# Performance work log

Measured on AMD Instinct MI355X. Metric: run time of the kernel, lower is better.

Reference implementation:

```python
import jax, jax.numpy as jnp
import numpy as np

T, B, I, H = 2048, 64, 256, 256

def setup_inputs() -> dict:
    key = jax.random.key(0)
    ks = jax.random.split(key, 9)
    s = 1.0 / np.sqrt(H)  # PyTorch RNN init scale (uniform(-s, s))
    u = lambda k, shape: jax.random.uniform(k, shape, jnp.float32, -s, s)
    return {
        "x": jax.random.normal(ks[0], (T, B, I), jnp.float32),
        "W_ih0": u(ks[1], (H, I)), "W_hh0": u(ks[2], (H, H)),
        "b_ih0": u(ks[3], (H,)),   "b_hh0": u(ks[4], (H,)),
        "W_ih1": u(ks[5], (H, H)), "W_hh1": u(ks[6], (H, H)),
        "b_ih1": u(ks[7], (H,)),   "b_hh1": u(ks[8], (H,)),
    }

def _rnn_layer(x, W_ih, W_hh, b_ih, b_hh):
    # x: [T, B, Din] -> [T, B, H]; h_t = tanh(x_t W_ih^T + b_ih + h_{t-1} W_hh^T + b_hh)
    xp = jnp.einsum('tbi,hi->tbh', x, W_ih) + (b_ih + b_hh)  # precompute input GEMM
    h0 = jnp.zeros((x.shape[1], W_hh.shape[0]), x.dtype)
    def step(h, xt):
        h = jnp.tanh(xt + h @ W_hh.T)
        return h, h
    _, ys = jax.lax.scan(step, h0, xp)
    return ys

def reference(x, W_ih0, W_hh0, b_ih0, b_hh0, W_ih1, W_hh1, b_ih1, b_hh1):
    h1 = _rnn_layer(x, W_ih0, W_hh0, b_ih0, b_hh0)
    h2 = _rnn_layer(h1, W_ih1, W_hh1, b_ih1, b_hh1)
    return h2.reshape(-1, H)  # [T*B, H], matching out.view(-1, hidden_size)
```

## Files before the change

kernel.cpp:

```cpp
#include <hip/hip_runtime.h>
#include <cstdint>

#define T_STEPS 2048
#define HID 256

typedef _Float16 half8 __attribute__((ext_vector_type(8)));
typedef float f32x4 __attribute__((ext_vector_type(4)));

__device__ __forceinline__ float tanh_fast(float x){
  float e = __builtin_amdgcn_exp2f(x * 2.8853900817779268f);
  float r = __builtin_amdgcn_rcpf(e + 1.0f);
  return __builtin_fmaf(-2.0f, r, 1.0f);
}

__device__ __forceinline__ half8 cvt_frag8(const float* __restrict__ p){
  float4 a = *(const float4*)p;
  float4 b = *(const float4*)(p + 4);
  half8 h;
  h[0]=(_Float16)a.x; h[1]=(_Float16)a.y; h[2]=(_Float16)a.z; h[3]=(_Float16)a.w;
  h[4]=(_Float16)b.x; h[5]=(_Float16)b.y; h[6]=(_Float16)b.z; h[7]=(_Float16)b.w;
  return h;
}

__global__ __launch_bounds__(512, 2) void gemm_xp0(
    const float* __restrict__ x, const float* __restrict__ W,
    const float* __restrict__ b1, const float* __restrict__ b2,
    _Float16* __restrict__ xp)
{
  const int t = blockIdx.x, tid = threadIdx.x;
  const int gw = tid >> 6, l = tid & 63;
  const int ng = gw & 1, mg = gw >> 1;
  const int lm = l & 15, lq = l >> 4;

  half8 Af[4][8];
  #pragma unroll
  for (int mt4 = 0; mt4 < 4; ++mt4)
    #pragma unroll
    for (int kc = 0; kc < 8; ++kc)
      Af[mt4][kc] = cvt_frag8(W + (long)(mg*64 + mt4*16 + lm)*HID + kc*32 + lq*8);

  half8 Bf[2][8];
  #pragma unroll
  for (int nt = 0; nt < 2; ++nt)
    #pragma unroll
    for (int kc = 0; kc < 8; ++kc)
      Bf[nt][kc] = cvt_frag8(x + ((long)t*64 + ng*32 + nt*16 + lm)*HID + kc*32 + lq*8);

  f32x4 acc[4][2];
  #pragma unroll
  for (int mt4 = 0; mt4 < 4; ++mt4)
    #pragma unroll
    for (int nt = 0; nt < 2; ++nt)
      acc[mt4][nt] = (f32x4){0.f,0.f,0.f,0.f};

  #pragma unroll
  for (int kc = 0; kc < 8; ++kc)
    #pragma unroll
    for (int mt4 = 0; mt4 < 4; ++mt4)
      #pragma unroll
      for (int nt = 0; nt < 2; ++nt)
        acc[mt4][nt] = __builtin_amdgcn_mfma_f32_16x16x32_f16(
            Af[mt4][kc], Bf[nt][kc], acc[mt4][nt], 0, 0, 0);

  _Float16* chunk0 = xp + ((long)t*4 + ng*2)*4096;
  #pragma unroll
  for (int wp = 0; wp < 2; ++wp){
    const int h0a = mg*64 + (2*wp    )*16 + lq*4;
    const int h0b = mg*64 + (2*wp + 1)*16 + lq*4;
    float4 ba1 = *(const float4*)(b1 + h0a), ba2 = *(const float4*)(b2 + h0a);
    float4 bb1 = *(const float4*)(b1 + h0b), bb2 = *(const float4*)(b2 + h0b);
    #pragma unroll
    for (int nt = 0; nt < 2; ++nt){
      f32x4 v0 = acc[2*wp][nt], v1 = acc[2*wp+1][nt];
      union { _Float16 h[8]; uint4 u; } pk;
      pk.h[0]=(_Float16)(v0[0]+ba1.x+ba2.x); pk.h[1]=(_Float16)(v0[1]+ba1.y+ba2.y);
      pk.h[2]=(_Float16)(v0[2]+ba1.z+ba2.z); pk.h[3]=(_Float16)(v0[3]+ba1.w+ba2.w);
      pk.h[4]=(_Float16)(v1[0]+bb1.x+bb2.x); pk.h[5]=(_Float16)(v1[1]+bb1.y+bb2.y);
      pk.h[6]=(_Float16)(v1[2]+bb1.z+bb2.z); pk.h[7]=(_Float16)(v1[3]+bb1.w+bb2.w);
      *(uint4*)(chunk0 + nt*4096 + ((mg*2 + wp)*64 + l)*8) = pk.u;
    }
  }
}

__global__ __launch_bounds__(512, 2) void fused_rec(
    const _Float16* __restrict__ xp,
    const float* __restrict__ Whh0, const float* __restrict__ Wih1,
    const float* __restrict__ Whh1,
    const float* __restrict__ b1, const float* __restrict__ b2,
    _Float16* __restrict__ hout)
{
  __shared__ __align__(16) _Float16 h1b[2][16][264];
  __shared__ __align__(16) _Float16 h2b[2][16][264];
  const int bi = blockIdx.x, tid = threadIdx.x;
  const int w = tid >> 6, l = tid & 63;
  const int lm = l & 15, lq = l >> 4;

  for (int i = tid; i < 16*264; i += 512){
    (&h1b[1][0][0])[i] = (_Float16)0.f;
    (&h2b[1][0][0])[i] = (_Float16)0.f;
  }

  half8 A0[2][8], A1[2][8], A2[2][8];
  #pragma unroll
  for (int mt = 0; mt < 2; ++mt)
    #pragma unroll
    for (int kc = 0; kc < 8; ++kc){
      const long r = (long)(w*32 + mt*16 + lm)*HID + kc*32 + lq*8;
      A0[mt][kc] = cvt_frag8(Whh0 + r);
      A1[mt][kc] = cvt_frag8(Wih1 + r);
      A2[mt][kc] = cvt_frag8(Whh1 + r);
    }

  f32x4 biasf[2];
  #pragma unroll
  for (int mt = 0; mt < 2; ++mt){
    const int h0 = w*32 + mt*16 + lq*4;
    f32x4 b;
    b[0]=b1[h0+0]+b2[h0+0]; b[1]=b1[h0+1]+b2[h0+1];
    b[2]=b1[h0+2]+b2[h0+2]; b[3]=b1[h0+3]+b2[h0+3];
    biasf[mt] = b;
  }
  __syncthreads();

  const _Float16* xptr = xp + (long)bi*4096 + (w*64 + l)*8;
  uint4 xv = *(const uint4*)xptr;
  _Float16* hob = hout + ((long)bi*16 + lm)*HID + w*32 + lq*4;

  for (int t = 0; t < T_STEPS; ++t){
    const int pb = (t + 1) & 1, cb = t & 1;

    union { uint4 u; _Float16 h[8]; } xu; xu.u = xv;
    f32x4 a0, a1;
    a0[0]=(float)xu.h[0]; a0[1]=(float)xu.h[1]; a0[2]=(float)xu.h[2]; a0[3]=(float)xu.h[3];
    a1[0]=(float)xu.h[4]; a1[1]=(float)xu.h[5]; a1[2]=(float)xu.h[6]; a1[3]=(float)xu.h[7];

    if (t + 1 < T_STEPS){ xptr += 4*4096; xv = *(const uint4*)xptr; }

    #pragma unroll
    for (int kc = 0; kc < 8; ++kc){
      half8 B = *(const half8*)&h1b[pb][lm][kc*32 + lq*8];
      a0 = __builtin_amdgcn_mfma_f32_16x16x32_f16(A0[0][kc], B, a0, 0,0,0);
      a1 = __builtin_amdgcn_mfma_f32_16x16x32_f16(A0[1][kc], B, a1, 0,0,0);
    }

    {
      union { _Float16 h[4]; uint64_t u; } p0, p1;
      p0.h[0]=(_Float16)tanh_fast(a0[0]); p0.h[1]=(_Float16)tanh_fast(a0[1]);
      p0.h[2]=(_Float16)tanh_fast(a0[2]); p0.h[3]=(_Float16)tanh_fast(a0[3]);
      p1.h[0]=(_Float16)tanh_fast(a1[0]); p1.h[1]=(_Float16)tanh_fast(a1[1]);
      p1.h[2]=(_Float16)tanh_fast(a1[2]); p1.h[3]=(_Float16)tanh_fast(a1[3]);
      *(uint64_t*)&h1b[cb][lm][w*32      + lq*4] = p0.u;
      *(uint64_t*)&h1b[cb][lm][w*32 + 16 + lq*4] = p1.u;
    }
    __syncthreads();

    a0 = biasf[0]; a1 = biasf[1];
    #pragma unroll
    for (int kc = 0; kc < 8; ++kc){
      half8 B = *(const half8*)&h1b[cb][lm][kc*32 + lq*8];
      a0 = __builtin_amdgcn_mfma_f32_16x16x32_f16(A1[0][kc], B, a0, 0,0,0);
      a1 = __builtin_amdgcn_mfma_f32_16x16x32_f16(A1[1][kc], B, a1, 0,0,0);
    }
    #pragma unroll
    for (int kc = 0; kc < 8; ++kc){
      half8 B = *(const half8*)&h2b[pb][lm][kc*32 + lq*8];
      a0 = __builtin_amdgcn_mfma_f32_16x16x32_f16(A2[0][kc], B, a0, 0,0,0);
      a1 = __builtin_amdgcn_mfma_f32_16x16x32_f16(A2[1][kc], B, a1, 0,0,0);
    }

    {
      union { _Float16 h[4]; uint64_t u; } q0, q1;
      q0.h[0]=(_Float16)tanh_fast(a0[0]); q0.h[1]=(_Float16)tanh_fast(a0[1]);
      q0.h[2]=(_Float16)tanh_fast(a0[2]); q0.h[3]=(_Float16)tanh_fast(a0[3]);
      q1.h[0]=(_Float16)tanh_fast(a1[0]); q1.h[1]=(_Float16)tanh_fast(a1[1]);
      q1.h[2]=(_Float16)tanh_fast(a1[2]); q1.h[3]=(_Float16)tanh_fast(a1[3]);
      *(uint64_t*)&h2b[cb][lm][w*32      + lq*4] = q0.u;
      *(uint64_t*)&h2b[cb][lm][w*32 + 16 + lq*4] = q1.u;
      _Float16* o = hob + (long)t*64*HID;
      *(uint64_t*)o        = q0.u;
      *(uint64_t*)(o + 16) = q1.u;
    }
    __syncthreads();
  }
}

__global__ __launch_bounds__(256) void cvt_out(
    const _Float16* __restrict__ hin, float* __restrict__ out)
{
  const long i = ((long)blockIdx.x*256 + threadIdx.x)*8;
  half8 v = *(const half8*)(hin + i);
  float4 a, b;
  a.x=(float)v[0]; a.y=(float)v[1]; a.z=(float)v[2]; a.w=(float)v[3];
  b.x=(float)v[4]; b.y=(float)v[5]; b.z=(float)v[6]; b.w=(float)v[7];
  *(float4*)(out + i)     = a;
  *(float4*)(out + i + 4) = b;
}

extern "C" void kernel_launch(void* const* d_in, const int* in_sizes, int n_in,
                              void* d_out, int out_size, void* d_ws, size_t ws_size,
                              hipStream_t stream)
{
  const float* x     = (const float*)d_in[0];
  const float* W_ih0 = (const float*)d_in[1];
  const float* W_hh0 = (const float*)d_in[2];
  const float* b_ih0 = (const float*)d_in[3];
  const float* b_hh0 = (const float*)d_in[4];
  const float* W_ih1 = (const float*)d_in[5];
  const float* W_hh1 = (const float*)d_in[6];
  const float* b_ih1 = (const float*)d_in[7];
  const float* b_hh1 = (const float*)d_in[8];

  _Float16* xp0 = (_Float16*)d_out;
  _Float16* h2  = (_Float16*)d_ws;

  gemm_xp0<<<T_STEPS, 512, 0, stream>>>(x, W_ih0, b_ih0, b_hh0, xp0);
  fused_rec<<<4, 512, 0, stream>>>(xp0, W_hh0, W_ih1, W_hh1, b_ih1, b_hh1, h2);
  cvt_out<<<(T_STEPS*64*HID)/(256*8), 256, 0, stream>>>(h2, (float*)d_out);
}
```

Baseline: 3.574 ms.

## Split the two RNN layers into producer/consumer blocks pipelined through global-memory flags

The fused recurrence kernel is split across 8 blocks. Blocks 0-3 run layer 0 only: four warps compute the recurrence while four others publish each step's hidden state into the spent xp slot and set a release flag. Blocks 4-7 run layer 1, spin on the flag and prefetch the next layer-0 state. The aim is to overlap the two serial recurrences instead of running both per step in one block, which shortens the per-step critical path. The cost is cross-block spin-wait synchronisation, and progress relies on all 8 blocks being resident at the same time.

```diff
diff --git a/kernel.cpp b/kernel.cpp
--- a/kernel.cpp
+++ b/kernel.cpp
@@ -3,6 +3,7 @@
 
 #define T_STEPS 2048
 #define HID 256
+#define TSTRIDE 16384
 
 typedef _Float16 half8 __attribute__((ext_vector_type(8)));
 typedef float f32x4 __attribute__((ext_vector_type(4)));
@@ -82,105 +83,184 @@
   }
 }
 
-__global__ __launch_bounds__(512, 2) void fused_rec(
-    const _Float16* __restrict__ xp,
+__global__ __launch_bounds__(512, 2) void fused_pipe(
+    _Float16* __restrict__ xp,
     const float* __restrict__ Whh0, const float* __restrict__ Wih1,
     const float* __restrict__ Whh1,
     const float* __restrict__ b1, const float* __restrict__ b2,
+    unsigned long long* __restrict__ flags,
     _Float16* __restrict__ hout)
 {
-  __shared__ __align__(16) _Float16 h1b[2][16][264];
-  __shared__ __align__(16) _Float16 h2b[2][16][264];
-  const int bi = blockIdx.x, tid = threadIdx.x;
+  __shared__ __align__(16) _Float16 hsb[2][16][264];
+  const int tid = threadIdx.x;
   const int w = tid >> 6, l = tid & 63;
   const int lm = l & 15, lq = l >> 4;
 
-  for (int i = tid; i < 16*264; i += 512){
-    (&h1b[1][0][0])[i] = (_Float16)0.f;
-    (&h2b[1][0][0])[i] = (_Float16)0.f;
-  }
-
-  half8 A0[2][8], A1[2][8], A2[2][8];
-  #pragma unroll
-  for (int mt = 0; mt < 2; ++mt)
+  for (int i = tid; i < 16*264; i += 512) (&hsb[1][0][0])[i] = (_Float16)0.f;
+
+  if (blockIdx.x < 4) {
+    const int bi = blockIdx.x;
+    unsigned long long* flag = flags + (size_t)bi*16;
+    _Float16* chunk0 = xp + (size_t)bi*4096;
+
+    if (w < 4) {
+      half8 A0[4][8];
+      #pragma unroll
+      for (int mt = 0; mt < 4; ++mt)
+        #pragma unroll
+        for (int kc = 0; kc < 8; ++kc)
+          A0[mt][kc] = cvt_frag8(Whh0 + (size_t)(w*64 + mt*16 + lm)*HID + kc*32 + lq*8);
+      __syncthreads();
+
+      uint4 xva = *(const uint4*)(chunk0 + ((2*w    )*64 + l)*8);
+      uint4 xvb = *(const uint4*)(chunk0 + ((2*w + 1)*64 + l)*8);
+
+      for (int t = 0; t <= T_STEPS; ++t){
+        const int pb = (t + 1) & 1, cb = t & 1;
+        if (t < T_STEPS){
+          union { uint4 u; _Float16 h[8]; } xa, xb;
+          xa.u = xva; xb.u = xvb;
+          f32x4 acc[4];
+          acc[0][0]=(float)xa.h[0]; acc[0][1]=(float)xa.h[1]; acc[0][2]=(float)xa.h[2]; acc[0][3]=(float)xa.h[3];
+          acc[1][0]=(float)xa.h[4]; acc[1][1]=(float)xa.h[5]; acc[1][2]=(float)xa.h[6]; acc[1][3]=(float)xa.h[7];
+          acc[2][0]=(float)xb.h[0]; acc[2][1]=(float)xb.h[1]; acc[2][2]=(float)xb.h[2]; acc[2][3]=(float)xb.h[3];
+          acc[3][0]=(float)xb.h[4]; acc[3][1]=(float)xb.h[5]; acc[3][2]=(float)xb.h[6]; acc[3][3]=(float)xb.h[7];
+
+          if (t + 1 < T_STEPS){
+            const _Float16* nx = chunk0 + (size_t)(t+1)*TSTRIDE;
+            xva = *(const uint4*)(nx + ((2*w    )*64 + l)*8);
+            xvb = *(const uint4*)(nx + ((2*w + 1)*64 + l)*8);
+          }
+
+          #pragma unroll
+          for (int kc = 0; kc < 8; ++kc){
+            half8 B = *(const half8*)&hsb[pb][lm][kc*32 + lq*8];
+            acc[0] = __builtin_amdgcn_mfma_f32_16x16x32_f16(A0[0][kc], B, acc[0], 0,0,0);
+            acc[1] = __builtin_amdgcn_mfma_f32_16x16x32_f16(A0[1][kc], B, acc[1], 0,0,0);
+            acc[2] = __builtin_amdgcn_mfma_f32_16x16x32_f16(A0[2][kc], B, acc[2], 0,0,0);
+            acc[3] = __builtin_amdgcn_mfma_f32_16x16x32_f16(A0[3][kc], B, acc[3], 0,0,0);
+          }
+
+          #pragma unroll
+          for (int mt = 0; mt < 4; ++mt){
+            union { _Float16 h[4]; unsigned long long u; } p;
+            p.h[0]=(_Float16)tanh_fast(acc[mt][0]); p.h[1]=(_Float16)tanh_fast(acc[mt][1]);
+            p.h[2]=(_Float16)tanh_fast(acc[mt][2]); p.h[3]=(_Float16)tanh_fast(acc[mt][3]);
+            *(unsigned long long*)&hsb[cb][lm][w*64 + mt*16 + lq*4] = p.u;
+          }
+        }
+        __syncthreads();
+      }
+    } else {
+      __syncthreads();
+      const int kcA = w - 4;
+      for (int t = 0; t <= T_STEPS; ++t){
+        const int pb = (t + 1) & 1;
+        if (t > 0){
+          union { half8 h; unsigned long long q[2]; } fa, fb;
+          fa.h = *(const half8*)&hsb[pb][lm][kcA*32 + lq*8];
+          fb.h = *(const half8*)&hsb[pb][lm][(kcA+4)*32 + lq*8];
+          _Float16* slot = chunk0 + (size_t)(t-1)*TSTRIDE;
+          unsigned long long* dA = (unsigned long long*)(slot + ((size_t)kcA*64 + l)*8);
+          unsigned long long* dB = (unsigned long long*)(slot + ((size_t)(kcA+4)*64 + l)*8);
+          __hip_atomic_store(dA,   fa.q[0], __ATOMIC_RELAXED, __HIP_MEMORY_SCOPE_AGENT);
+          __hip_atomic_store(dA+1, fa.q[1], __ATOMIC_RELAXED, __HIP_MEMORY_SCOPE_AGENT);
+          __hip_atomic_store(dB,   fb.q[0], __ATOMIC_RELAXED, __HIP_MEMORY_SCOPE_AGENT);
+          __hip_atomic_store(dB+1, fb.q[1], __ATOMIC_RELAXED, __HIP_MEMORY_SCOPE_AGENT);
+        }
+        __syncthreads();
+        if (tid == 256 && t > 0)
+          __hip_atomic_store(flag, (unsigned long long)t,
+                             __ATOMIC_RELEASE, __HIP_MEMORY_SCOPE_AGENT);
+      }
+    }
+  } else {
+    const int bi = blockIdx.x - 4;
+    const unsigned long long* flag = flags + (size_t)bi*16;
+    const _Float16* chunk0 = xp + (size_t)bi*4096;
+
+    half8 A1[2][8], A2[2][8];
+    #pragma unroll
+    for (int mt = 0; mt < 2; ++mt)
+      #pragma unroll
+      for (int kc = 0; kc < 8; ++kc){
+        const size_t r = (size_t)(w*32 + mt*16 + lm)*HID + kc*32 + lq*8;
+        A1[mt][kc] = cvt_frag8(Wih1 + r);
+        A2[mt][kc] = cvt_frag8(Whh1 + r);
+      }
+    f32x4 biasf[2];
+    #pragma unroll
+    for (int mt = 0; mt < 2; ++mt){
+      const int h0 = w*32 + mt*16 + lq*4;
+      f32x4 b;
+      b[0]=b1[h0+0]+b2[h0+0]; b[1]=b1[h0+1]+b2[h0+1];
+      b[2]=b1[h0+2]+b2[h0+2]; b[3]=b1[h0+3]+b2[h0+3];
+      biasf[mt] = b;
+    }
+    __syncthreads();
+    _Float16* hob = hout + ((size_t)bi*16 + lm)*HID + w*32 + lq*4;
+
+    while (__hip_atomic_load(flag, __ATOMIC_ACQUIRE, __HIP_MEMORY_SCOPE_AGENT) < 1ull)
+      __builtin_amdgcn_s_sleep(2);
+    half8 pfc[8], pfn[8];
     #pragma unroll
     for (int kc = 0; kc < 8; ++kc){
-      const long r = (long)(w*32 + mt*16 + lm)*HID + kc*32 + lq*8;
-      A0[mt][kc] = cvt_frag8(Whh0 + r);
-      A1[mt][kc] = cvt_frag8(Wih1 + r);
-      A2[mt][kc] = cvt_frag8(Whh1 + r);
-    }
-
-  f32x4 biasf[2];
-  #pragma unroll
-  for (int mt = 0; mt < 2; ++mt){
-    const int h0 = w*32 + mt*16 + lq*4;
-    f32x4 b;
-    b[0]=b1[h0+0]+b2[h0+0]; b[1]=b1[h0+1]+b2[h0+1];
-    b[2]=b1[h0+2]+b2[h0+2]; b[3]=b1[h0+3]+b2[h0+3];
-    biasf[mt] = b;
-  }
-  __syncthreads();
-
-  const _Float16* xptr = xp + (long)bi*4096 + (w*64 + l)*8;
-  uint4 xv = *(const uint4*)xptr;
-  _Float16* hob = hout + ((long)bi*16 + lm)*HID + w*32 + lq*4;
-
-  for (int t = 0; t < T_STEPS; ++t){
-    const int pb = (t + 1) & 1, cb = t & 1;
-
-    union { uint4 u; _Float16 h[8]; } xu; xu.u = xv;
-    f32x4 a0, a1;
-    a0[0]=(float)xu.h[0]; a0[1]=(float)xu.h[1]; a0[2]=(float)xu.h[2]; a0[3]=(float)xu.h[3];
-    a1[0]=(float)xu.h[4]; a1[1]=(float)xu.h[5]; a1[2]=(float)xu.h[6]; a1[3]=(float)xu.h[7];
-
-    if (t + 1 < T_STEPS){ xptr += 4*4096; xv = *(const uint4*)xptr; }
-
-    #pragma unroll
-    for (int kc = 0; kc < 8; ++kc){
-      half8 B = *(const half8*)&h1b[pb][lm][kc*32 + lq*8];
-      a0 = __builtin_amdgcn_mfma_f32_16x16x32_f16(A0[0][kc], B, a0, 0,0,0);
-      a1 = __builtin_amdgcn_mfma_f32_16x16x32_f16(A0[1][kc], B, a1, 0,0,0);
-    }
-
-    {
-      union { _Float16 h[4]; uint64_t u; } p0, p1;
-      p0.h[0]=(_Float16)tanh_fast(a0[0]); p0.h[1]=(_Float16)tanh_fast(a0[1]);
-      p0.h[2]=(_Float16)tanh_fast(a0[2]); p0.h[3]=(_Float16)tanh_fast(a0[3]);
-      p1.h[0]=(_Float16)tanh_fast(a1[0]); p1.h[1]=(_Float16)tanh_fast(a1[1]);
-      p1.h[2]=(_Float16)tanh_fast(a1[2]); p1.h[3]=(_Float16)tanh_fast(a1[3]);
-      *(uint64_t*)&h1b[cb][lm][w*32      + lq*4] = p0.u;
-      *(uint64_t*)&h1b[cb][lm][w*32 + 16 + lq*4] = p1.u;
-    }
-    __syncthreads();
-
-    a0 = biasf[0]; a1 = biasf[1];
-    #pragma unroll
-    for (int kc = 0; kc < 8; ++kc){
-      half8 B = *(const half8*)&h1b[cb][lm][kc*32 + lq*8];
-      a0 = __builtin_amdgcn_mfma_f32_16x16x32_f16(A1[0][kc], B, a0, 0,0,0);
-      a1 = __builtin_amdgcn_mfma_f32_16x16x32_f16(A1[1][kc], B, a1, 0,0,0);
-    }
-    #pragma unroll
-    for (int kc = 0; kc < 8; ++kc){
-      half8 B = *(const half8*)&h2b[pb][lm][kc*32 + lq*8];
-      a0 = __builtin_amdgcn_mfma_f32_16x16x32_f16(A2[0][kc], B, a0, 0,0,0);
-      a1 = __builtin_amdgcn_mfma_f32_16x16x32_f16(A2[1][kc], B, a1, 0,0,0);
-    }
-
-    {
-      union { _Float16 h[4]; uint64_t u; } q0, q1;
+      const unsigned long long* s = (const unsigned long long*)(chunk0 + ((size_t)kc*64 + l)*8);
+      union { half8 h; unsigned long long q[2]; } u;
+      u.q[0] = __hip_atomic_load(s,   __ATOMIC_RELAXED, __HIP_MEMORY_SCOPE_AGENT);
+      u.q[1] = __hip_atomic_load(s+1, __ATOMIC_RELAXED, __HIP_MEMORY_SCOPE_AGENT);
+      pfc[kc] = u.h;
+    }
+
+    for (int t = 0; t < T_STEPS; ++t){
+      const int pb = (t + 1) & 1, cb = t & 1;
+      f32x4 a0 = biasf[0], a1 = biasf[1];
+
+      #pragma unroll
+      for (int kc = 0; kc < 8; ++kc){
+        a0 = __builtin_amdgcn_mfma_f32_16x16x32_f16(A1[0][kc], pfc[kc], a0, 0,0,0);
+        a1 = __builtin_amdgcn_mfma_f32_16x16x32_f16(A1[1][kc], pfc[kc], a1, 0,0,0);
+      }
+
+      if (t + 1 < T_STEPS){
+        while (__hip_atomic_load(flag, __ATOMIC_ACQUIRE, __HIP_MEMORY_SCOPE_AGENT)
+               < (unsigned long long)(t + 2))
+          __builtin_amdgcn_s_sleep(2);
+        const _Float16* slot = chunk0 + (size_t)(t+1)*TSTRIDE;
+        #pragma unroll
+        for (int kc = 0; kc < 8; ++kc){
+          const unsigned long long* s = (const unsigned long long*)(slot + ((size_t)kc*64 + l)*8);
+          union { half8 h; unsigned long long q[2]; } u;
+          u.q[0] = __hip_atomic_load(s,   __ATOMIC_RELAXED, __HIP_MEMORY_SCOPE_AGENT);
+          u.q[1] = __hip_atomic_load(s+1, __ATOMIC_RELAXED, __HIP_MEMORY_SCOPE_AGENT);
+          pfn[kc] = u.h;
+        }
+      }
+
+      #pragma unroll
+      for (int kc = 0; kc < 8; ++kc){
+        half8 B = *(const half8*)&hsb[pb][lm][kc*32 + lq*8];
+        a0 = __builtin_amdgcn_mfma_f32_16x16x32_f16(A2[0][kc], B, a0, 0,0,0);
+        a1 = __builtin_amdgcn_mfma_f32_16x16x32_f16(A2[1][kc], B, a1, 0,0,0);
+      }
+
+      union { _Float16 h[4]; unsigned long long u; } q0, q1;
       q0.h[0]=(_Float16)tanh_fast(a0[0]); q0.h[1]=(_Float16)tanh_fast(a0[1]);
       q0.h[2]=(_Float16)tanh_fast(a0[2]); q0.h[3]=(_Float16)tanh_fast(a0[3]);
       q1.h[0]=(_Float16)tanh_fast(a1[0]); q1.h[1]=(_Float16)tanh_fast(a1[1]);
       q1.h[2]=(_Float16)tanh_fast(a1[2]); q1.h[3]=(_Float16)tanh_fast(a1[3]);
-      *(uint64_t*)&h2b[cb][lm][w*32      + lq*4] = q0.u;
-      *(uint64_t*)&h2b[cb][lm][w*32 + 16 + lq*4] = q1.u;
-      _Float16* o = hob + (long)t*64*HID;
-      *(uint64_t*)o        = q0.u;
-      *(uint64_t*)(o + 16) = q1.u;
-    }
-    __syncthreads();
+      *(unsigned long long*)&hsb[cb][lm][w*32      + lq*4] = q0.u;
+      *(unsigned long long*)&hsb[cb][lm][w*32 + 16 + lq*4] = q1.u;
+      _Float16* o = hob + (size_t)t*64*HID;
+      *(unsigned long long*)o        = q0.u;
+      *(unsigned long long*)(o + 16) = q1.u;
+      __syncthreads();
+
+      if (t + 1 < T_STEPS){
+        #pragma unroll
+        for (int kc = 0; kc < 8; ++kc) pfc[kc] = pfn[kc];
+      }
+    }
   }
 }
 
@@ -211,9 +291,13 @@
   const float* b_hh1 = (const float*)d_in[8];
 
   _Float16* xp0 = (_Float16*)d_out;
+  unsigned long long* flags =
+      (unsigned long long*)((char*)d_out + (size_t)T_STEPS*64*HID*2);
   _Float16* h2  = (_Float16*)d_ws;
 
   gemm_xp0<<<T_STEPS, 512, 0, stream>>>(x, W_ih0, b_ih0, b_hh0, xp0);
-  fused_rec<<<4, 512, 0, stream>>>(xp0, W_hh0, W_ih1, W_hh1, b_ih1, b_hh1, h2);
+  hipMemsetAsync(flags, 0, 1024, stream);
+  fused_pipe<<<8, 512, 0, stream>>>(xp0, W_hh0, W_ih1, W_hh1, b_ih1, b_hh1,
+                                    flags, h2);
   cvt_out<<<(T_STEPS*64*HID)/(256*8), 256, 0, stream>>>(h2, (float*)d_out);
 }
```

After: 5.336 ms. +49.3%, slower.

## Use 4 waves with 64 rows each and fragment-ordered LDS hidden state

Applied to the files above, without the earlier changes.

The recurrent kernel drops from 8 to 4 waves per block, with each wave owning 64 hidden rows (4 MFMA tiles), so each B fragment read from shared memory is reused across 4 tiles. The hidden-state buffers are stored in MFMA fragment order so a lane reads its B fragment contiguously. The layer-2 W_hh1·h2 product is interleaved with the layer-1 product before the barrier, moving it off the critical path. The risk is much higher register pressure (96 weight fragments per thread) and fewer waves to hide latency on the serial chain.

```diff
diff --git a/kernel.cpp b/kernel.cpp
--- a/kernel.cpp
+++ b/kernel.cpp
@@ -3,6 +3,7 @@
 
 #define T_STEPS 2048
 #define HID 256
+#define TSTRIDE 16384
 
 typedef _Float16 half8 __attribute__((ext_vector_type(8)));
 typedef float f32x4 __attribute__((ext_vector_type(4)));
@@ -82,39 +83,39 @@
   }
 }
 
-__global__ __launch_bounds__(512, 2) void fused_rec(
+__global__ __launch_bounds__(256, 1) void fused_rec(
     const _Float16* __restrict__ xp,
     const float* __restrict__ Whh0, const float* __restrict__ Wih1,
     const float* __restrict__ Whh1,
     const float* __restrict__ b1, const float* __restrict__ b2,
     _Float16* __restrict__ hout)
 {
-  __shared__ __align__(16) _Float16 h1b[2][16][264];
-  __shared__ __align__(16) _Float16 h2b[2][16][264];
+  __shared__ __align__(16) _Float16 h1f[2][8][64][8];
+  __shared__ __align__(16) _Float16 h2f[2][8][64][8];
   const int bi = blockIdx.x, tid = threadIdx.x;
   const int w = tid >> 6, l = tid & 63;
   const int lm = l & 15, lq = l >> 4;
 
-  for (int i = tid; i < 16*264; i += 512){
-    (&h1b[1][0][0])[i] = (_Float16)0.f;
-    (&h2b[1][0][0])[i] = (_Float16)0.f;
-  }
-
-  half8 A0[2][8], A1[2][8], A2[2][8];
-  #pragma unroll
-  for (int mt = 0; mt < 2; ++mt)
+  for (int i = tid; i < 8*64*8; i += 256){
+    (&h1f[1][0][0][0])[i] = (_Float16)0.f;
+    (&h2f[1][0][0][0])[i] = (_Float16)0.f;
+  }
+
+  half8 A0[4][8], A1[4][8], A2[4][8];
+  #pragma unroll
+  for (int mt = 0; mt < 4; ++mt)
     #pragma unroll
     for (int kc = 0; kc < 8; ++kc){
-      const long r = (long)(w*32 + mt*16 + lm)*HID + kc*32 + lq*8;
+      const size_t r = (size_t)(w*64 + mt*16 + lm)*HID + kc*32 + lq*8;
       A0[mt][kc] = cvt_frag8(Whh0 + r);
       A1[mt][kc] = cvt_frag8(Wih1 + r);
       A2[mt][kc] = cvt_frag8(Whh1 + r);
     }
 
-  f32x4 biasf[2];
-  #pragma unroll
-  for (int mt = 0; mt < 2; ++mt){
-    const int h0 = w*32 + mt*16 + lq*4;
+  f32x4 biasf[4];
+  #pragma unroll
+  for (int mt = 0; mt < 4; ++mt){
+    const int h0 = w*64 + mt*16 + lq*4;
     f32x4 b;
     b[0]=b1[h0+0]+b2[h0+0]; b[1]=b1[h0+1]+b2[h0+1];
     b[2]=b1[h0+2]+b2[h0+2]; b[3]=b1[h0+3]+b2[h0+3];
@@ -122,63 +123,70 @@
   }
   __syncthreads();
 
-  const _Float16* xptr = xp + (long)bi*4096 + (w*64 + l)*8;
-  uint4 xv = *(const uint4*)xptr;
-  _Float16* hob = hout + ((long)bi*16 + lm)*HID + w*32 + lq*4;
+  const _Float16* chunk0 = xp + (size_t)bi*4096;
+  uint4 xva = *(const uint4*)(chunk0 + ((2*w    )*64 + l)*8);
+  uint4 xvb = *(const uint4*)(chunk0 + ((2*w + 1)*64 + l)*8);
+
+  _Float16* hob = hout + ((size_t)bi*16 + lm)*HID + w*64 + lq*4;
 
   for (int t = 0; t < T_STEPS; ++t){
     const int pb = (t + 1) & 1, cb = t & 1;
 
-    union { uint4 u; _Float16 h[8]; } xu; xu.u = xv;
-    f32x4 a0, a1;
-    a0[0]=(float)xu.h[0]; a0[1]=(float)xu.h[1]; a0[2]=(float)xu.h[2]; a0[3]=(float)xu.h[3];
-    a1[0]=(float)xu.h[4]; a1[1]=(float)xu.h[5]; a1[2]=(float)xu.h[6]; a1[3]=(float)xu.h[7];
-
-    if (t + 1 < T_STEPS){ xptr += 4*4096; xv = *(const uint4*)xptr; }
+    union { uint4 u; _Float16 h[8]; } xa, xb;
+    xa.u = xva; xb.u = xvb;
+    f32x4 acc1[4], acc2[4];
+    acc1[0][0]=(float)xa.h[0]; acc1[0][1]=(float)xa.h[1]; acc1[0][2]=(float)xa.h[2]; acc1[0][3]=(float)xa.h[3];
+    acc1[1][0]=(float)xa.h[4]; acc1[1][1]=(float)xa.h[5]; acc1[1][2]=(float)xa.h[6]; acc1[1][3]=(float)xa.h[7];
+    acc1[2][0]=(float)xb.h[0]; acc1[2][1]=(float)xb.h[1]; acc1[2][2]=(float)xb.h[2]; acc1[2][3]=(float)xb.h[3];
+    acc1[3][0]=(float)xb.h[4]; acc1[3][1]=(float)xb.h[5]; acc1[3][2]=(float)xb.h[6]; acc1[3][3]=(float)xb.h[7];
+    #pragma unroll
+    for (int mt = 0; mt < 4; ++mt) acc2[mt] = biasf[mt];
+
+    if (t + 1 < T_STEPS){
+      const _Float16* nx = chunk0 + (size_t)(t+1)*TSTRIDE;
+      xva = *(const uint4*)(nx + ((2*w    )*64 + l)*8);
+      xvb = *(const uint4*)(nx + ((2*w + 1)*64 + l)*8);
+    }
 
     #pragma unroll
     for (int kc = 0; kc < 8; ++kc){
-      half8 B = *(const half8*)&h1b[pb][lm][kc*32 + lq*8];
-      a0 = __builtin_amdgcn_mfma_f32_16x16x32_f16(A0[0][kc], B, a0, 0,0,0);
-      a1 = __builtin_amdgcn_mfma_f32_16x16x32_f16(A0[1][kc], B, a1, 0,0,0);
-    }
-
-    {
-      union { _Float16 h[4]; uint64_t u; } p0, p1;
-      p0.h[0]=(_Float16)tanh_fast(a0[0]); p0.h[1]=(_Float16)tanh_fast(a0[1]);
-      p0.h[2]=(_Float16)tanh_fast(a0[2]); p0.h[3]=(_Float16)tanh_fast(a0[3]);
-      p1.h[0]=(_Float16)tanh_fast(a1[0]); p1.h[1]=(_Float16)tanh_fast(a1[1]);
-      p1.h[2]=(_Float16)tanh_fast(a1[2]); p1.h[3]=(_Float16)tanh_fast(a1[3]);
-      *(uint64_t*)&h1b[cb][lm][w*32      + lq*4] = p0.u;
-      *(uint64_t*)&h1b[cb][lm][w*32 + 16 + lq*4] = p1.u;
+      half8 B0 = *(const half8*)&h1f[pb][kc][l][0];
+      half8 B2 = *(const half8*)&h2f[pb][kc][l][0];
+      #pragma unroll
+      for (int mt = 0; mt < 4; ++mt){
+        acc1[mt] = __builtin_amdgcn_mfma_f32_16x16x32_f16(A0[mt][kc], B0, acc1[mt], 0,0,0);
+        acc2[mt] = __builtin_amdgcn_mfma_f32_16x16x32_f16(A2[mt][kc], B2, acc2[mt], 0,0,0);
+      }
+    }
+
+    #pragma unroll
+    for (int mt = 0; mt < 4; ++mt){
+      union { _Float16 h[4]; unsigned long long u; } p;
+      p.h[0]=(_Float16)tanh_fast(acc1[mt][0]); p.h[1]=(_Float16)tanh_fast(acc1[mt][1]);
+      p.h[2]=(_Float16)tanh_fast(acc1[mt][2]); p.h[3]=(_Float16)tanh_fast(acc1[mt][3]);
+      const int kcd = 2*w + (mt>>1);
+      const int lp  = lm + 16*((mt&1)*2 + (lq>>1));
+      *(unsigned long long*)&h1f[cb][kcd][lp][(lq&1)*4] = p.u;
     }
     __syncthreads();
 
-    a0 = biasf[0]; a1 = biasf[1];
     #pragma unroll
     for (int kc = 0; kc < 8; ++kc){
-      half8 B = *(const half8*)&h1b[cb][lm][kc*32 + lq*8];
-      a0 = __builtin_amdgcn_mfma_f32_16x16x32_f16(A1[0][kc], B, a0, 0,0,0);
-      a1 = __builtin_amdgcn_mfma_f32_16x16x32_f16(A1[1][kc], B, a1, 0,0,0);
-    }
-    #pragma unroll
-    for (int kc = 0; kc < 8; ++kc){
-      half8 B = *(const half8*)&h2b[pb][lm][kc*32 + lq*8];
-      a0 = __builtin_amdgcn_mfma_f32_16x16x32_f16(A2[0][kc], B, a0, 0,0,0);
-      a1 = __builtin_amdgcn_mfma_f32_16x16x32_f16(A2[1][kc], B, a1, 0,0,0);
-    }
-
-    {
-      union { _Float16 h[4]; uint64_t u; } q0, q1;
-      q0.h[0]=(_Float16)tanh_fast(a0[0]); q0.h[1]=(_Float16)tanh_fast(a0[1]);
-      q0.h[2]=(_Float16)tanh_fast(a0[2]); q0.h[3]=(_Float16)tanh_fast(a0[3]);
-      q1.h[0]=(_Float16)tanh_fast(a1[0]); q1.h[1]=(_Float16)tanh_fast(a1[1]);
-      q1.h[2]=(_Float16)tanh_fast(a1[2]); q1.h[3]=(_Float16)tanh_fast(a1[3]);
-      *(uint64_t*)&h2b[cb][lm][w*32      + lq*4] = q0.u;
-      *(uint64_t*)&h2b[cb][lm][w*32 + 16 + lq*4] = q1.u;
-      _Float16* o = hob + (long)t*64*HID;
-      *(uint64_t*)o        = q0.u;
-      *(uint64_t*)(o + 16) = q1.u;
+      half8 B1 = *(const half8*)&h1f[cb][kc][l][0];
+      #pragma unroll
+      for (int mt = 0; mt < 4; ++mt)
+        acc2[mt] = __builtin_amdgcn_mfma_f32_16x16x32_f16(A1[mt][kc], B1, acc2[mt], 0,0,0);
+    }
+
+    #pragma unroll
+    for (int mt = 0; mt < 4; ++mt){
+      union { _Float16 h[4]; unsigned long long u; } q;
+      q.h[0]=(_Float16)tanh_fast(acc2[mt][0]); q.h[1]=(_Float16)tanh_fast(acc2[mt][1]);
+      q.h[2]=(_Float16)tanh_fast(acc2[mt][2]); q.h[3]=(_Float16)tanh_fast(acc2[mt][3]);
+      const int kcd = 2*w + (mt>>1);
+      const int lp  = lm + 16*((mt&1)*2 + (lq>>1));
+      *(unsigned long long*)&h2f[cb][kcd][lp][(lq&1)*4] = q.u;
+      *(unsigned long long*)(hob + (size_t)t*64*HID + mt*16) = q.u;
     }
     __syncthreads();
   }
@@ -214,6 +222,6 @@
   _Float16* h2  = (_Float16*)d_ws;
 
   gemm_xp0<<<T_STEPS, 512, 0, stream>>>(x, W_ih0, b_ih0, b_hh0, xp0);
-  fused_rec<<<4, 512, 0, stream>>>(xp0, W_hh0, W_ih1, W_hh1, b_ih1, b_hh1, h2);
+  fused_rec<<<4, 256, 0, stream>>>(xp0, W_hh0, W_ih1, W_hh1, b_ih1, b_hh1, h2);
   cvt_out<<<(T_STEPS*64*HID)/(256*8), 256, 0, stream>>>(h2, (float*)d_out);
 }
```

Result: slower. 5.089 ms (+42.4%).
